# Performance work log

Measured on AMD Instinct MI355X. Metric: run time of the kernel, lower is better.

## Reference

```python
import jax, jax.numpy as jnp
import numpy as np

NODE, HIDDEN, BATCH, OUT, BUF = 200, 10, 50, 64, 500
DT = 0.0001
# ParamsJR('JR') defaults (all variances 0 -> constants, not Parameters)
A_, a_, B_, b_ = 3.25, 100.0, 22.0, 50.0
g_, c1_, c2_, c3_, c4_ = 1000.0, 135.0, 135.0 * 0.8, 135.0 * 0.25, 135.0 * 0.25
std_in_, vmax, v0, r_, y0, cy0 = 100.0, 5.0, 6.0, 0.56, 2.0, 5.0
LB, U_UB, NOISE_LB, SAT = 0.01, 500.0, 150.0, 1000.0


def setup_inputs() -> dict:
    key = jax.random.key(0)
    ks = jax.random.split(key, 8)
    inp = jax.random.normal(ks[0], (NODE, HIDDEN, BATCH), dtype=jnp.float32)
    noise_in = jax.random.normal(ks[1], (NODE, HIDDEN, BATCH), dtype=jnp.float32)
    hx = jax.random.uniform(ks[2], (NODE, 6), dtype=jnp.float32)
    hE = jax.random.uniform(ks[3], (NODE, BUF), dtype=jnp.float32)
    sc = jax.random.uniform(ks[4], (NODE, NODE), dtype=jnp.float32)
    w_bb = jax.random.uniform(ks[5], (NODE, NODE), dtype=jnp.float32)  # fitted gains (init 0.05 in torch)
    lm = jax.random.normal(ks[6], (OUT, NODE), dtype=jnp.float32)  # lead-field
    delays = jax.random.randint(ks[7], (NODE, NODE), 0, BUF)  # (dist/(1.5+relu(mu))).int64
    return {"inp": inp, "noise_in": noise_in, "hx": hx, "hE": hE,
            "sc": sc, "w_bb": w_bb, "lm": lm, "delays": delays}


def _sigmoid(x):
    return vmax / (1.0 + jnp.exp(r_ * (v0 - x)))


def _sys2nd(A, a, u, x, v):
    return A * a * u - 2.0 * a * v - a * a * x


def _forward(inp, noise_in, hx, hE, sc, w_bb, lm, delays):
    relu = jax.nn.relu
    A_e, a_e = relu(A_), 1.0 + relu(a_)          # 0*con+relu(A), 1*con+relu(a)
    B_e, b_e = relu(B_), 1.0 + relu(b_)
    g_e, c1e, c2e, c3e, c4e = (LB + relu(g_), LB + relu(c1_), LB + relu(c2_),
                               LB + relu(c3_), LB + relu(c4_))
    std_e = NOISE_LB + relu(std_in_)

    # normalized laplacian-style connectivity
    w = jnp.exp(w_bb) * sc
    wl = jnp.log1p(0.5 * (w + w.T))
    w_n = wl / jnp.linalg.norm(wl)
    dg = -jnp.diag(jnp.sum(w_n, axis=1))          # (node, node)
    rows = jnp.arange(NODE)[:, None]

    def step(carry, xs):
        M, E, I, Mv, Ev, Iv, hEb = carry
        u, noise = xs                              # (node,1) each
        Ed = hEb[rows, delays]                     # Ed[i,j] = hE[i, delays[i,j]]
        LEd = jnp.sum(w_n * Ed.T, axis=1, keepdims=True)  # (node,1)
        rM = _sigmoid(E - I)
        rE = (std_e * noise + g_e * (LEd + dg @ E)
              + c2e * _sigmoid(c1e * M))
        rI = c4e * _sigmoid(c3e * M)
        ddM = M + DT * Mv
        ddE = E + DT * Ev
        ddI = I + DT * Iv
        ddMv = Mv + DT * _sys2nd(A_e, a_e, u + U_UB * jnp.tanh(rM / U_UB), M, Mv)
        ddEv = Ev + DT * _sys2nd(A_e, a_e, U_UB * jnp.tanh(rE / U_UB), E, Ev)
        ddIv = Iv + DT * _sys2nd(B_e, b_e, U_UB * jnp.tanh(rI / U_UB), I, Iv)
        sat = lambda x: SAT * jnp.tanh(x / SAT)
        M, E, I, Mv, Ev, Iv = (sat(ddM), sat(ddE), sat(ddI),
                               sat(ddMv), sat(ddEv), sat(ddIv))
        hEb = jnp.concatenate([M, hEb[:, :-1]], axis=1)  # push pyramidal state into delay buffer
        return (M, E, I, Mv, Ev, Iv, hEb), None

    def tr_step(carry, xs):
        u_tr, n_tr = xs                            # (hidden, node, 1)
        carry, _ = jax.lax.scan(step, carry, (u_tr, n_tr))
        M, E, I, Mv, Ev, Iv, _ = carry
        return carry, (M[:, 0], E[:, 0], I[:, 0], Mv[:, 0], Ev[:, 0], Iv[:, 0])

    M, E, I = hx[:, 0:1], hx[:, 1:2], hx[:, 2:3]
    Mv, Ev, Iv = hx[:, 3:4], hx[:, 4:5], hx[:, 5:6]
    u_all = jnp.transpose(inp, (2, 1, 0))[..., None]       # (batch, hidden, node, 1)
    n_all = jnp.transpose(noise_in, (2, 1, 0))[..., None]
    carry, recs = jax.lax.scan(tr_step, (M, E, I, Mv, Ev, Iv, hE), (u_all, n_all))
    Mb, Eb, Ib, Mvb, Evb, Ivb = recs                       # (batch, node) each

    # lead-field: row-normalize then remove channel mean
    lm_n = lm / jnp.sqrt(jnp.sum(lm ** 2, axis=1, keepdims=True))
    lm_t = lm_n - jnp.mean(lm_n, axis=0, keepdims=True)
    eeg = cy0 * jnp.einsum('on,bn->ob', lm_t, Eb - Ib) - y0  # (output, batch)

    M, E, I, Mv, Ev, Iv, hEb = carry
    current_state = jnp.concatenate([M, E, I, Mv, Ev, Iv], axis=1)
    return eeg, current_state, Eb.T, Ib.T, Mb.T, Evb.T, Ivb.T, Mvb.T, hEb


def reference(inp, noise_in, hx, hE, sc, w_bb, lm, delays):
    return _forward(inp, noise_in, hx, hE, sc, w_bb, lm, delays)
```

## Files before the change

### kernel.cpp

```cpp
#include <hip/hip_runtime.h>
#include <math.h>

#define N_NODE 200
#define RING   512
#define ROWF   545
#define NSTEP  500
#define TB     32
#define NB     16
#define NWG    8
#define NTHR   256
#define JSL    25
#define NEARCAP 32
#define MDEP   36
#define MSZ    (MDEP * N_NODE)

#define FPBUF   (NWG * N_NODE * TB)
#define OFF_FP  0
#define OFF_BAR (2 * FPBUF)
#define WS_NEED ((size_t)(2 * FPBUF + 64) * 4)

#define SM_RED   0
#define SM_MREC  64
#define SM_US    28864
#define SM_NS    54464
#define SM_LED   80864
#define SM_RING  106464
#define SM_TOTAL 160964
#define SM_LMT   64
#define SM_DIFF  51264

__device__ __forceinline__ float ftanh(float x) {
    float ax = fabsf(x);
    float t  = __expf(-2.0f * ax);
    float r  = __fdividef(1.0f - t, 1.0f + t);
    return copysignf(r, x);
}
__device__ __forceinline__ float sigm(float x) {
    return __fdividef(5.0f, 1.0f + __expf(0.56f * (6.0f - x)));
}
__device__ __forceinline__ float satf(float x) {
    return 1000.0f * ftanh(x * 0.001f);
}

__device__ __forceinline__ void grid_barrier(int* slot, int nwg) {
    __syncthreads();
    if (threadIdx.x == 0) {
        __threadfence();
        __hip_atomic_fetch_add(slot, 1, __ATOMIC_ACQ_REL, __HIP_MEMORY_SCOPE_AGENT);
        while (__hip_atomic_load(slot, __ATOMIC_ACQUIRE, __HIP_MEMORY_SCOPE_AGENT) < nwg) {
            __builtin_amdgcn_s_sleep(2);
        }
        __threadfence();
    }
    __syncthreads();
}

__global__ void zero_bar(int* bar) {
    if (threadIdx.x < 64) bar[threadIdx.x] = 0;
}

__global__ __launch_bounds__(NTHR, 1)
void jansen_pg(const float* __restrict__ inp, const float* __restrict__ noise_in,
               const float* __restrict__ hx,  const float* __restrict__ hE,
               const float* __restrict__ sc,  const float* __restrict__ wbb,
               const float* __restrict__ lm,  const int*   __restrict__ delays,
               float* __restrict__ out, float* __restrict__ ws)
{
    __shared__ char smem[SM_TOTAL];
    double*   red  = (double*)(smem + SM_RED);
    float*    Mrec = (float*)(smem + SM_MREC);
    unsigned* n1OFF = (unsigned*)(smem + SM_US);
    float*    n1W   = (float*)(smem + SM_NS);
    unsigned* n0J   = (unsigned*)(smem + SM_LED);
    float*    n0W   = (float*)(smem + SM_LED + 8 * N_NODE * 4);
    float*    uS   = (float*)(smem + SM_US);
    float*    nS   = (float*)(smem + SM_NS);
    float*    LEdS = (float*)(smem + SM_LED);
    float*    ringS= (float*)(smem + SM_RING);

    const int tid = threadIdx.x;
    const int wg  = blockIdx.x;
    const int i   = tid;
    const int jlo = wg * JSL;

    float* fp  = ws + OFF_FP;
    int*   bar = (int*)(ws + OFF_BAR);

    double ssq = 0.0;
    for (int q = tid; q < N_NODE * N_NODE; q += NTHR) {
        int j = q / N_NODE, ii = q - j * N_NODE;
        float w1 = expf(wbb[ii * N_NODE + j]) * sc[ii * N_NODE + j];
        float w2 = expf(wbb[j * N_NODE + ii]) * sc[j * N_NODE + ii];
        float wl = log1pf(0.5f * (w1 + w2));
        ssq += (double)wl * (double)wl;
    }
    #pragma unroll
    for (int off = 32; off > 0; off >>= 1) ssq += __shfl_down(ssq, off, 64);
    if ((tid & 63) == 0) red[tid >> 6] = ssq;

    for (int p = tid; p < JSL * ROWF; p += NTHR) {
        int jl = p / ROWF, x = p - jl * ROWF;
        float v = 0.0f;
        if (x < 544) {
            int dd = (x < RING) ? (511 - x) : (1023 - x);
            if (dd < 500) v = hE[(jlo + jl) * 500 + dd];
        }
        ringS[p] = v;
    }
    for (int p = tid; p < MDEP * N_NODE; p += NTHR) {
        int s = p / N_NODE, j = p - s * N_NODE;
        Mrec[p] = (s >= 4) ? hE[j * 500 + (35 - s)] : 0.0f;
    }
    for (int p = tid; p < 32 * N_NODE; p += NTHR) {
        n1OFF[p] = 0u;
        n1W[p]   = 0.0f;
    }
    for (int p = tid; p < 8 * N_NODE; p += NTHR) {
        n0J[p] = 0u;
        n0W[p] = 0.0f;
    }
    __syncthreads();
    if (tid == 0) {
        double s = 0.0;
        #pragma unroll
        for (int r = 0; r < 8; ++r) s += red[r];
        red[0] = 1.0 / sqrt(s);
    }
    __syncthreads();
    const float inv = (float)red[0];

    float rowsum = 0.0f;
    float M = 0, E = 0, I = 0, Mvv = 0, Evv = 0, Ivv = 0;
    float wreg[JSL];
    int   ereg[JSL];
    #pragma unroll
    for (int jl = 0; jl < JSL; ++jl) { wreg[jl] = 0.0f; ereg[jl] = 0; }
    int cnt0 = 0, cnt1 = 0;
    if (i < N_NODE) {
        for (int j = 0; j < N_NODE; ++j) {
            float w1 = expf(wbb[i * N_NODE + j]) * sc[i * N_NODE + j];
            float w2 = expf(wbb[j * N_NODE + i]) * sc[j * N_NODE + i];
            float w  = log1pf(0.5f * (w1 + w2)) * inv;
            int d = delays[j * N_NODE + i];
            rowsum += w;
            if (d == 0) {
                if (cnt0 < 8) {
                    n0J[cnt0 * N_NODE + i] = (unsigned)j;
                    n0W[cnt0 * N_NODE + i] = w;
                    ++cnt0;
                }
            } else if (d < NEARCAP) {
                if (cnt1 < 32) {
                    n1OFF[cnt1 * N_NODE + i] = (unsigned)((35 - d) * N_NODE + j);
                    n1W  [cnt1 * N_NODE + i] = w;
                    ++cnt1;
                }
            }
        }
        #pragma unroll
        for (int jl = 0; jl < JSL; ++jl) {
            int j = jlo + jl;
            float w1 = expf(wbb[i * N_NODE + j]) * sc[i * N_NODE + j];
            float w2 = expf(wbb[j * N_NODE + i]) * sc[j * N_NODE + i];
            float w  = log1pf(0.5f * (w1 + w2)) * inv;
            int d = delays[j * N_NODE + i];
            wreg[jl] = (d < NEARCAP) ? 0.0f : w;
            ereg[jl] = 511 - d;
        }
        M   = hx[i * 6 + 0]; E   = hx[i * 6 + 1]; I   = hx[i * 6 + 2];
        Mvv = hx[i * 6 + 3]; Evv = hx[i * 6 + 4]; Ivv = hx[i * 6 + 5];
    }

    int   n1off[32]; float n1w[32];
    int   n0j[8];    float n0w[8];
    {
        const int ii = (i < N_NODE) ? i : 0;
        #pragma unroll
        for (int n = 0; n < 32; ++n) {
            n1off[n] = (int)n1OFF[n * N_NODE + ii];
            n1w[n]   = n1W[n * N_NODE + ii];
        }
        #pragma unroll
        for (int z = 0; z < 8; ++z) {
            n0j[z] = (int)n0J[z * N_NODE + ii];
            n0w[z] = n0W[z * N_NODE + ii];
        }
    }

    float LEdN = 0.0f;
    if (i < N_NODE) {
        float gA = 0.0f, gB = 0.0f, gC = 0.0f, gD = 0.0f;
        #pragma unroll
        for (int n = 0; n < 8; ++n) gA = fmaf(n1w[n], Mrec[n1off[n]], gA);
        if (cnt1 > 8) {
            #pragma unroll
            for (int n = 8; n < 16; ++n) gB = fmaf(n1w[n], Mrec[n1off[n]], gB);
        }
        if (cnt1 > 16) {
            #pragma unroll
            for (int n = 16; n < 24; ++n) gC = fmaf(n1w[n], Mrec[n1off[n]], gC);
        }
        if (cnt1 > 24) {
            #pragma unroll
            for (int n = 24; n < 32; ++n) gD = fmaf(n1w[n], Mrec[n1off[n]], gD);
        }
        LEdN = (gA + gB) + (gC + gD);
    }
    __syncthreads();

    int base36 = 0;
    for (int b = 0; b < NB; ++b) {
        const int t0 = b * TB;
        float* fpb = fp + (b & 1) * FPBUF;

        if (i < N_NODE) {
            float ac[TB];
            #pragma unroll
            for (int k = 0; k < TB; ++k) ac[k] = 0.0f;
            #pragma unroll
            for (int jl = 0; jl < JSL; ++jl) {
                float w  = wreg[jl];
                int   p0 = (t0 + ereg[jl]) & 511;
                const float* rb = ringS + jl * ROWF + p0;
                #pragma unroll
                for (int k = 0; k < TB; ++k)
                    ac[k] = fmaf(w, rb[k], ac[k]);
            }
            float4* fpw = (float4*)(fpb + wg * (N_NODE * TB) + i * TB);
            #pragma unroll
            for (int q = 0; q < 8; ++q)
                fpw[q] = make_float4(ac[4*q+0], ac[4*q+1], ac[4*q+2], ac[4*q+3]);

            #pragma unroll
            for (int k = 0; k < TB; ++k) {
                int t = t0 + k;
                float uv = 0.0f, nv = 0.0f;
                if (t < NSTEP) {
                    int bb = t / 10, h = t - 10 * bb;
                    uv = inp     [i * 500 + h * 50 + bb];
                    nv = noise_in[i * 500 + h * 50 + bb];
                }
                uS[k * N_NODE + i] = uv;
                nS[k * N_NODE + i] = nv;
            }
        }

        grid_barrier(bar + b, NWG);

        if (i < N_NODE) {
            const float* basep = fpb + i * TB;
            #pragma unroll
            for (int c = 0; c < 8; ++c) {
                float sx = 0, sy = 0, sz = 0, sw = 0;
                #pragma unroll
                for (int g = 0; g < NWG; ++g) {
                    float4 q = *(const float4*)(basep + g * (N_NODE * TB) + c * 4);
                    sx += q.x; sy += q.y; sz += q.z; sw += q.w;
                }
                LEdS[(c * 4 + 0) * N_NODE + i] = sx;
                LEdS[(c * 4 + 1) * N_NODE + i] = sy;
                LEdS[(c * 4 + 2) * N_NODE + i] = sz;
                LEdS[(c * 4 + 3) * N_NODE + i] = sw;
            }
        }
        __syncthreads();

        const int kmax = (NSTEP - t0 < TB) ? (NSTEP - t0) : TB;
        int bcur = t0 / 10, hcur = t0 - 10 * bcur;
        const bool ringw = (i >= jlo) && (i < jlo + JSL);
        const int  rbase = (i - jlo) * ROWF;
        for (int k = 0; k < kmax; ++k) {
            const int t = t0 + k;
            if (i < N_NODE) {
                const int base_prev = (base36 == 0) ? (MSZ - N_NODE) : (base36 - N_NODE);
                float LEd = LEdN + LEdS[k * N_NODE + i];
                float u  = uS[k * N_NODE + i];
                float nz = nS[k * N_NODE + i];
                #pragma unroll
                for (int z = 0; z < 4; ++z)
                    LEd = fmaf(n0w[z], Mrec[base_prev + n0j[z]], LEd);
                if (cnt0 > 4) {
                    #pragma unroll
                    for (int z = 4; z < 8; ++z)
                        LEd = fmaf(n0w[z], Mrec[base_prev + n0j[z]], LEd);
                }
                int base36n = base36 + N_NODE; if (base36n == MSZ) base36n = 0;
                float gA = 0.0f, gB = 0.0f, gC = 0.0f, gD = 0.0f;
                #pragma unroll
                for (int n = 0; n < 8; ++n) {
                    int a = base36n + n1off[n]; if (a >= MSZ) a -= MSZ;
                    gA = fmaf(n1w[n], Mrec[a], gA);
                }
                if (cnt1 > 8) {
                    #pragma unroll
                    for (int n = 8; n < 16; ++n) {
                        int a = base36n + n1off[n]; if (a >= MSZ) a -= MSZ;
                        gB = fmaf(n1w[n], Mrec[a], gB);
                    }
                }
                if (cnt1 > 16) {
                    #pragma unroll
                    for (int n = 16; n < 24; ++n) {
                        int a = base36n + n1off[n]; if (a >= MSZ) a -= MSZ;
                        gC = fmaf(n1w[n], Mrec[a], gC);
                    }
                }
                if (cnt1 > 24) {
                    #pragma unroll
                    for (int n = 24; n < 32; ++n) {
                        int a = base36n + n1off[n]; if (a >= MSZ) a -= MSZ;
                        gD = fmaf(n1w[n], Mrec[a], gD);
                    }
                }
                float rM = sigm(E - I);
                float rE = 250.0f * nz + 1000.01f * (LEd - rowsum * E) + 108.01f * sigm(135.01f * M);
                float rI = 33.76f * sigm(33.76f * M);
                float ddM = M + 1e-4f * Mvv;
                float ddE = E + 1e-4f * Evv;
                float ddI = I + 1e-4f * Ivv;
                float uu  = u + 500.0f * ftanh(rM * 0.002f);
                float ddMv = Mvv + 1e-4f * (328.25f * uu - 202.0f * Mvv - 10201.0f * M);
                float uE  = 500.0f * ftanh(rE * 0.002f);
                float ddEv = Evv + 1e-4f * (328.25f * uE - 202.0f * Evv - 10201.0f * E);
                float uI  = 500.0f * ftanh(rI * 0.002f);
                float ddIv = Ivv + 1e-4f * (1122.0f * uI - 102.0f * Ivv - 2601.0f * I);
                M   = satf(ddM);  E   = satf(ddE);  I   = satf(ddI);
                Mvv = satf(ddMv); Evv = satf(ddEv); Ivv = satf(ddIv);
                LEdN = (gA + gB) + (gC + gD);
                Mrec[base36 + i] = M;
                if (ringw) {
                    int pt = t & 511;
                    ringS[rbase + pt] = M;
                    if (pt < 32) ringS[rbase + pt + 512] = M;
                }
                if (wg == 0 && hcur == 9) {
                    out[ 4400 + i * 50 + bcur] = E;
                    out[14400 + i * 50 + bcur] = I;
                    out[24400 + i * 50 + bcur] = M;
                    out[34400 + i * 50 + bcur] = Evv;
                    out[44400 + i * 50 + bcur] = Ivv;
                    out[54400 + i * 50 + bcur] = Mvv;
                }
                ++hcur; if (hcur == 10) { hcur = 0; ++bcur; }
                base36 = base36n;
            }
            __syncthreads();
        }
    }

    for (int p = tid; p < JSL * 500; p += NTHR) {
        int jl = p / 500, dd = p - jl * 500;
        out[64400 + (jlo + jl) * 500 + dd] = ringS[jl * ROWF + ((499 - dd) & 511)];
    }
    if (wg != 0) return;

    if (i < N_NODE) {
        out[3200 + i * 6 + 0] = M;
        out[3200 + i * 6 + 1] = E;
        out[3200 + i * 6 + 2] = I;
        out[3200 + i * 6 + 3] = Mvv;
        out[3200 + i * 6 + 4] = Evv;
        out[3200 + i * 6 + 5] = Ivv;
    }

    float* lmt  = (float*)(smem + SM_LMT);
    float* diff = (float*)(smem + SM_DIFF);
    __syncthreads();
    if (tid < 64) {
        float s = 0.0f;
        for (int n = 0; n < N_NODE; ++n) { float v = lm[tid * N_NODE + n]; s += v * v; }
        float ivn = 1.0f / sqrtf(s);
        for (int n = 0; n < N_NODE; ++n) lmt[tid * N_NODE + n] = lm[tid * N_NODE + n] * ivn;
    }
    __syncthreads();
    if (tid < N_NODE) {
        float s = 0.0f;
        for (int o = 0; o < 64; ++o) s += lmt[o * N_NODE + tid];
        s *= (1.0f / 64.0f);
        for (int o = 0; o < 64; ++o) lmt[o * N_NODE + tid] -= s;
    }
    __syncthreads();
    for (int p = tid; p < 10000; p += NTHR) diff[p] = out[4400 + p] - out[14400 + p];
    __syncthreads();
    for (int p = tid; p < 3200; p += NTHR) {
        int o = p / 50, bb = p - o * 50;
        float s = 0.0f;
        for (int n = 0; n < N_NODE; ++n)
            s = fmaf(lmt[o * N_NODE + n], diff[n * 50 + bb], s);
        out[p] = 5.0f * s - 2.0f;
    }
}

__global__ __launch_bounds__(1024, 1)
void jansen_main(const float* __restrict__ inp, const float* __restrict__ noise_in,
                 const float* __restrict__ hx,  const float* __restrict__ hE,
                 const float* __restrict__ sc,  const float* __restrict__ wbb,
                 const float* __restrict__ lm,  const int*   __restrict__ delays,
                 float* __restrict__ out, float* __restrict__ ws)
{
    const int tid = threadIdx.x;
    const int i   = tid & 255;
    const int c   = tid >> 8;

    float* ring = ws;
    float* lmt  = ws + N_NODE * RING;

    __shared__ double red[18];
    __shared__ float  part[4][N_NODE];
    __shared__ float  wn[N_NODE * N_NODE];

    double ssq = 0.0;
    for (int p = tid; p < N_NODE * N_NODE; p += 1024) {
        int r0 = p / N_NODE;
        int cc = p - r0 * N_NODE;
        float w1 = expf(wbb[p]) * sc[p];
        float w2 = expf(wbb[cc * N_NODE + r0]) * sc[cc * N_NODE + r0];
        float v  = log1pf(0.5f * (w1 + w2));
        wn[p] = v;
        ssq += (double)v * (double)v;
    }
    #pragma unroll
    for (int off = 32; off > 0; off >>= 1) ssq += __shfl_down(ssq, off, 64);
    if ((tid & 63) == 0) red[tid >> 6] = ssq;
    __syncthreads();
    if (tid == 0) {
        double s = 0.0;
        for (int k = 0; k < 16; ++k) s += red[k];
        red[16] = 1.0 / sqrt(s);
    }
    __syncthreads();
    const float inv_norm = (float)red[16];
    for (int p = tid; p < N_NODE * N_NODE; p += 1024) wn[p] *= inv_norm;

    for (int p = tid; p < N_NODE * 500; p += 1024) {
        int j = p / 500, dd = p - j * 500;
        ring[j * RING + (511 - dd)] = hE[p];
    }
    if (tid < 64) {
        float s = 0.0f;
        for (int n = 0; n < N_NODE; ++n) { float v = lm[tid * N_NODE + n]; s += v * v; }
        float inv = 1.0f / sqrtf(s);
        for (int n = 0; n < N_NODE; ++n) lmt[tid * N_NODE + n] = lm[tid * N_NODE + n] * inv;
    }
    __syncthreads();
    if (tid < N_NODE) {
        float s = 0.0f;
        for (int o = 0; o < 64; ++o) s += lmt[o * N_NODE + tid];
        s *= (1.0f / 64.0f);
        for (int o = 0; o < 64; ++o) lmt[o * N_NODE + tid] -= s;
    }

    unsigned int dpk[25];
    if (i < N_NODE) {
        #pragma unroll
        for (int r0 = 0; r0 < 25; ++r0) {
            int d0 = delays[(c * 50 + 2 * r0    ) * N_NODE + i];
            int d1 = delays[(c * 50 + 2 * r0 + 1) * N_NODE + i];
            unsigned e0 = (unsigned)((-1 - d0) & 511);
            unsigned e1 = (unsigned)((-1 - d1) & 511);
            dpk[r0] = e0 | (e1 << 16);
        }
    }

    float M = 0, E = 0, I = 0, Mvv = 0, Evv = 0, Ivv = 0, rowsum = 0;
    if (c == 0 && i < N_NODE) {
        M   = hx[i * 6 + 0]; E   = hx[i * 6 + 1]; I   = hx[i * 6 + 2];
        Mvv = hx[i * 6 + 3]; Evv = hx[i * 6 + 4]; Ivv = hx[i * 6 + 5];
    }
    __syncthreads();
    if (c == 0 && i < N_NODE) {
        float s = 0.0f;
        for (int j = 0; j < N_NODE; ++j) s += wn[j * N_NODE + i];
        rowsum = s;
    }

    for (int t = 0; t < NSTEP; ++t) {
        if (i < N_NODE) {
            float acc = 0.0f;
            const float* ringc = ring + c * 50 * RING;
            const float* wnc   = wn + c * 50 * N_NODE + i;
            #pragma unroll
            for (int r0 = 0; r0 < 50; ++r0) {
                unsigned e = (dpk[r0 >> 1] >> ((r0 & 1) << 4)) & 0xffffu;
                int pos = (int)(((unsigned)t + e) & 511u);
                acc = fmaf(wnc[r0 * N_NODE], ringc[r0 * RING + pos], acc);
            }
            part[c][i] = acc;
        }
        __syncthreads();
        if (c == 0 && i < N_NODE) {
            float LEd = part[0][i] + part[1][i] + part[2][i] + part[3][i];
            int b = t / 10, h = t - b * 10;
            float u  = inp     [i * 500 + h * 50 + b];
            float nz = noise_in[i * 500 + h * 50 + b];
            float rM = 5.0f / (1.0f + expf(0.56f * (6.0f - (E - I))));
            float rE = 250.0f * nz + 1000.01f * (LEd - rowsum * E) + 108.01f * (5.0f / (1.0f + expf(0.56f * (6.0f - 135.01f * M))));
            float rI = 33.76f * (5.0f / (1.0f + expf(0.56f * (6.0f - 33.76f * M))));
            float ddM = M + 1e-4f * Mvv;
            float ddE = E + 1e-4f * Evv;
            float ddI = I + 1e-4f * Ivv;
            float uu  = u + 500.0f * tanhf(rM / 500.0f);
            float ddMv = Mvv + 1e-4f * (328.25f * uu - 202.0f * Mvv - 10201.0f * M);
            float uE  = 500.0f * tanhf(rE / 500.0f);
            float ddEv = Evv + 1e-4f * (328.25f * uE - 202.0f * Evv - 10201.0f * E);
            float uI  = 500.0f * tanhf(rI / 500.0f);
            float ddIv = Ivv + 1e-4f * (1122.0f * uI - 102.0f * Ivv - 2601.0f * I);
            M   = 1000.0f * tanhf(ddM / 1000.0f);
            E   = 1000.0f * tanhf(ddE / 1000.0f);
            I   = 1000.0f * tanhf(ddI / 1000.0f);
            Mvv = 1000.0f * tanhf(ddMv / 1000.0f);
            Evv = 1000.0f * tanhf(ddEv / 1000.0f);
            Ivv = 1000.0f * tanhf(ddIv / 1000.0f);
            ring[i * RING + (t & 511)] = M;
            if (h == 9) {
                out[ 4400 + i * 50 + b] = E;
                out[14400 + i * 50 + b] = I;
                out[24400 + i * 50 + b] = M;
                out[34400 + i * 50 + b] = Evv;
                out[44400 + i * 50 + b] = Ivv;
                out[54400 + i * 50 + b] = Mvv;
            }
        }
        __syncthreads();
    }

    if (c == 0 && i < N_NODE) {
        out[3200 + i * 6 + 0] = M;
        out[3200 + i * 6 + 1] = E;
        out[3200 + i * 6 + 2] = I;
        out[3200 + i * 6 + 3] = Mvv;
        out[3200 + i * 6 + 4] = Evv;
        out[3200 + i * 6 + 5] = Ivv;
    }
    for (int p = tid; p < N_NODE * 500; p += 1024) {
        int ii = p / 500, dd = p - ii * 500;
        out[64400 + p] = ring[ii * RING + (499 - dd)];
    }
    __syncthreads();
    for (int p = tid; p < 64 * 50; p += 1024) {
        int o = p / 50, b = p - o * 50;
        float s = 0.0f;
        for (int n = 0; n < N_NODE; ++n)
            s += lmt[o * N_NODE + n] * (out[4400 + n * 50 + b] - out[14400 + n * 50 + b]);
        out[p] = 5.0f * s - 2.0f;
    }
}

extern "C" void kernel_launch(void* const* d_in, const int* in_sizes, int n_in,
                              void* d_out, int out_size, void* d_ws, size_t ws_size,
                              hipStream_t stream) {
    if (ws_size >= WS_NEED) {
        zero_bar<<<1, 64, 0, stream>>>((int*)((float*)d_ws + OFF_BAR));
        jansen_pg<<<NWG, NTHR, 0, stream>>>(
            (const float*)d_in[0], (const float*)d_in[1], (const float*)d_in[2],
            (const float*)d_in[3], (const float*)d_in[4], (const float*)d_in[5],
            (const float*)d_in[6], (const int*)d_in[7],
            (float*)d_out, (float*)d_ws);
    } else {
        jansen_main<<<1, 1024, 0, stream>>>(
            (const float*)d_in[0], (const float*)d_in[1], (const float*)d_in[2],
            (const float*)d_in[3], (const float*)d_in[4], (const float*)d_in[5],
            (const float*)d_in[6], (const int*)d_in[7],
            (float*)d_out, (float*)d_ws);
    }
}
```

Before: 1.253 ms.

## Advance two timesteps per block barrier by recomputing zero-delay neighbor states locally

The inner time loop now runs two ODE steps between consecutive __syncthreads instead of one. For step t+1, the zero-delay neighbor term needs neighbor M at step t. That value is rebuilt locally as satf(M + 1e-4*Mv) from last-step M and Mv values kept in small shared double buffers, and the near-delay gathers for both steps are interleaved. The input and noise staging arrays are packed into float2, and the norm reduction now sums only the 4 wavefront partials that exist. This halves block synchronisations per step, at the cost of redundant neighbor recomputation and higher register pressure.

```diff
diff --git a/kernel.cpp b/kernel.cpp
--- a/kernel.cpp
+++ b/kernel.cpp
@@ -10,24 +10,30 @@
 #define NWG    8
 #define NTHR   256
 #define JSL    25
-#define NEARCAP 32
 #define MDEP   36
 #define MSZ    (MDEP * N_NODE)
+#define L1CAP  32
+#define L0CAP  8
 
 #define FPBUF   (NWG * N_NODE * TB)
 #define OFF_FP  0
 #define OFF_BAR (2 * FPBUF)
 #define WS_NEED ((size_t)(2 * FPBUF + 64) * 4)
 
-#define SM_RED   0
-#define SM_MREC  64
-#define SM_US    28864
-#define SM_NS    54464
-#define SM_LED   80864
-#define SM_RING  106464
-#define SM_TOTAL 160964
-#define SM_LMT   64
-#define SM_DIFF  51264
+#define SM_RED    0
+#define SM_MREC   64
+#define SM_MLAST  28864
+#define SM_MVLAST 30464
+#define SM_US     32064
+#define SM_LEDS   83264
+#define SM_RING   108864
+#define SM_TOTAL  163364
+#define SM_N1X    SM_US
+#define SM_N1W    (SM_US + 25600)
+#define SM_N0J    SM_LEDS
+#define SM_N0W    (SM_LEDS + 6400)
+#define SM_LMT    64
+#define SM_DIFF   51264
 
 __device__ __forceinline__ float ftanh(float x) {
     float ax = fabsf(x);
@@ -59,23 +65,41 @@
     if (threadIdx.x < 64) bar[threadIdx.x] = 0;
 }
 
+#define ODE_STEP(LEDV, UV, NZV) do { \
+    float rM = sigm(E - I); \
+    float rE = 250.0f * (NZV) + 1000.01f * ((LEDV) - rowsum * E) + 108.01f * sigm(135.01f * M); \
+    float rI = 33.76f * sigm(33.76f * M); \
+    float ddM = fmaf(1e-4f, Mvv, M); \
+    float ddE = fmaf(1e-4f, Evv, E); \
+    float ddI = fmaf(1e-4f, Ivv, I); \
+    float uu  = (UV) + 500.0f * ftanh(rM * 0.002f); \
+    float ddMv = Mvv + 1e-4f * (328.25f * uu - 202.0f * Mvv - 10201.0f * M); \
+    float uE  = 500.0f * ftanh(rE * 0.002f); \
+    float ddEv = Evv + 1e-4f * (328.25f * uE - 202.0f * Evv - 10201.0f * E); \
+    float uI  = 500.0f * ftanh(rI * 0.002f); \
+    float ddIv = Ivv + 1e-4f * (1122.0f * uI - 102.0f * Ivv - 2601.0f * I); \
+    M   = satf(ddM);  E   = satf(ddE);  I   = satf(ddI); \
+    Mvv = satf(ddMv); Evv = satf(ddEv); Ivv = satf(ddIv); \
+} while (0)
+
 __global__ __launch_bounds__(NTHR, 1)
-void jansen_pg(const float* __restrict__ inp, const float* __restrict__ noise_in,
+void jansen_2s(const float* __restrict__ inp, const float* __restrict__ noise_in,
                const float* __restrict__ hx,  const float* __restrict__ hE,
                const float* __restrict__ sc,  const float* __restrict__ wbb,
                const float* __restrict__ lm,  const int*   __restrict__ delays,
                float* __restrict__ out, float* __restrict__ ws)
 {
     __shared__ char smem[SM_TOTAL];
-    double*   red  = (double*)(smem + SM_RED);
-    float*    Mrec = (float*)(smem + SM_MREC);
-    unsigned* n1OFF = (unsigned*)(smem + SM_US);
-    float*    n1W   = (float*)(smem + SM_NS);
-    unsigned* n0J   = (unsigned*)(smem + SM_LED);
-    float*    n0W   = (float*)(smem + SM_LED + 8 * N_NODE * 4);
-    float*    uS   = (float*)(smem + SM_US);
-    float*    nS   = (float*)(smem + SM_NS);
-    float*    LEdS = (float*)(smem + SM_LED);
+    double*   red   = (double*)(smem + SM_RED);
+    float*    Mrec  = (float*)(smem + SM_MREC);
+    float*    Mlast = (float*)(smem + SM_MLAST);
+    float*    Mvlast= (float*)(smem + SM_MVLAST);
+    unsigned* n1X = (unsigned*)(smem + SM_N1X);
+    float*    n1W = (float*)(smem + SM_N1W);
+    unsigned* n0J = (unsigned*)(smem + SM_N0J);
+    float*    n0W = (float*)(smem + SM_N0W);
+    float2*   unS  = (float2*)(smem + SM_US);
+    float*    LEdS = (float*)(smem + SM_LEDS);
     float*    ringS= (float*)(smem + SM_RING);
 
     const int tid = threadIdx.x;
@@ -107,23 +131,17 @@
         }
         ringS[p] = v;
     }
-    for (int p = tid; p < MDEP * N_NODE; p += NTHR) {
+    for (int p = tid; p < MSZ; p += NTHR) {
         int s = p / N_NODE, j = p - s * N_NODE;
         Mrec[p] = (s >= 4) ? hE[j * 500 + (35 - s)] : 0.0f;
     }
-    for (int p = tid; p < 32 * N_NODE; p += NTHR) {
-        n1OFF[p] = 0u;
-        n1W[p]   = 0.0f;
-    }
-    for (int p = tid; p < 8 * N_NODE; p += NTHR) {
-        n0J[p] = 0u;
-        n0W[p] = 0.0f;
-    }
+    for (int p = tid; p < L1CAP * N_NODE; p += NTHR) { n1X[p] = 0u; n1W[p] = 0.0f; }
+    for (int p = tid; p < L0CAP * N_NODE; p += NTHR) { n0J[p] = 0u; n0W[p] = 0.0f; }
     __syncthreads();
     if (tid == 0) {
         double s = 0.0;
         #pragma unroll
-        for (int r = 0; r < 8; ++r) s += red[r];
+        for (int r = 0; r < 4; ++r) s += red[r];
         red[0] = 1.0 / sqrt(s);
     }
     __syncthreads();
@@ -144,15 +162,15 @@
             int d = delays[j * N_NODE + i];
             rowsum += w;
             if (d == 0) {
-                if (cnt0 < 8) {
+                if (cnt0 < L0CAP) {
                     n0J[cnt0 * N_NODE + i] = (unsigned)j;
                     n0W[cnt0 * N_NODE + i] = w;
                     ++cnt0;
                 }
-            } else if (d < NEARCAP) {
-                if (cnt1 < 32) {
-                    n1OFF[cnt1 * N_NODE + i] = (unsigned)((35 - d) * N_NODE + j);
-                    n1W  [cnt1 * N_NODE + i] = w;
+            } else if (d < 32) {
+                if (cnt1 < L1CAP) {
+                    n1X[cnt1 * N_NODE + i] = (unsigned)((35 - d) * N_NODE + j);
+                    n1W[cnt1 * N_NODE + i] = w;
                     ++cnt1;
                 }
             }
@@ -164,51 +182,32 @@
             float w2 = expf(wbb[j * N_NODE + i]) * sc[j * N_NODE + i];
             float w  = log1pf(0.5f * (w1 + w2)) * inv;
             int d = delays[j * N_NODE + i];
-            wreg[jl] = (d < NEARCAP) ? 0.0f : w;
+            wreg[jl] = (d < 32) ? 0.0f : w;
             ereg[jl] = 511 - d;
         }
         M   = hx[i * 6 + 0]; E   = hx[i * 6 + 1]; I   = hx[i * 6 + 2];
         Mvv = hx[i * 6 + 3]; Evv = hx[i * 6 + 4]; Ivv = hx[i * 6 + 5];
-    }
-
-    int   n1off[32]; float n1w[32];
-    int   n0j[8];    float n0w[8];
+        Mlast [N_NODE + i] = M;
+        Mvlast[N_NODE + i] = Mvv;
+    }
+
+    int   n1off[L1CAP]; float n1w[L1CAP];
+    int   l0j[L0CAP];   float l0w[L0CAP];
     {
         const int ii = (i < N_NODE) ? i : 0;
         #pragma unroll
-        for (int n = 0; n < 32; ++n) {
-            n1off[n] = (int)n1OFF[n * N_NODE + ii];
+        for (int n = 0; n < L1CAP; ++n) {
+            n1off[n] = (int)n1X[n * N_NODE + ii];
             n1w[n]   = n1W[n * N_NODE + ii];
         }
         #pragma unroll
-        for (int z = 0; z < 8; ++z) {
-            n0j[z] = (int)n0J[z * N_NODE + ii];
-            n0w[z] = n0W[z * N_NODE + ii];
-        }
-    }
-
-    float LEdN = 0.0f;
-    if (i < N_NODE) {
-        float gA = 0.0f, gB = 0.0f, gC = 0.0f, gD = 0.0f;
-        #pragma unroll
-        for (int n = 0; n < 8; ++n) gA = fmaf(n1w[n], Mrec[n1off[n]], gA);
-        if (cnt1 > 8) {
-            #pragma unroll
-            for (int n = 8; n < 16; ++n) gB = fmaf(n1w[n], Mrec[n1off[n]], gB);
-        }
-        if (cnt1 > 16) {
-            #pragma unroll
-            for (int n = 16; n < 24; ++n) gC = fmaf(n1w[n], Mrec[n1off[n]], gC);
-        }
-        if (cnt1 > 24) {
-            #pragma unroll
-            for (int n = 24; n < 32; ++n) gD = fmaf(n1w[n], Mrec[n1off[n]], gD);
-        }
-        LEdN = (gA + gB) + (gC + gD);
-    }
-    __syncthreads();
-
-    int base36 = 0;
+        for (int z = 0; z < L0CAP; ++z) {
+            l0j[z] = (int)n0J[z * N_NODE + ii];
+            l0w[z] = n0W[z * N_NODE + ii];
+        }
+    }
+    __syncthreads();
+
     for (int b = 0; b < NB; ++b) {
         const int t0 = b * TB;
         float* fpb = fp + (b & 1) * FPBUF;
@@ -240,8 +239,7 @@
                     uv = inp     [i * 500 + h * 50 + bb];
                     nv = noise_in[i * 500 + h * 50 + bb];
                 }
-                uS[k * N_NODE + i] = uv;
-                nS[k * N_NODE + i] = nv;
+                unS[k * N_NODE + i] = make_float2(uv, nv);
             }
         }
 
@@ -266,72 +264,75 @@
         __syncthreads();
 
         const int kmax = (NSTEP - t0 < TB) ? (NSTEP - t0) : TB;
+        int s36 = t0 % MDEP;
         int bcur = t0 / 10, hcur = t0 - 10 * bcur;
         const bool ringw = (i >= jlo) && (i < jlo + JSL);
         const int  rbase = (i - jlo) * ROWF;
-        for (int k = 0; k < kmax; ++k) {
-            const int t = t0 + k;
+        for (int k2 = 0; k2 < kmax; k2 += 2) {
+            const int t = t0 + k2;
             if (i < N_NODE) {
-                const int base_prev = (base36 == 0) ? (MSZ - N_NODE) : (base36 - N_NODE);
-                float LEd = LEdN + LEdS[k * N_NODE + i];
-                float u  = uS[k * N_NODE + i];
-                float nz = nS[k * N_NODE + i];
-                #pragma unroll
-                for (int z = 0; z < 4; ++z)
-                    LEd = fmaf(n0w[z], Mrec[base_prev + n0j[z]], LEd);
-                if (cnt0 > 4) {
-                    #pragma unroll
-                    for (int z = 4; z < 8; ++z)
-                        LEd = fmaf(n0w[z], Mrec[base_prev + n0j[z]], LEd);
-                }
-                int base36n = base36 + N_NODE; if (base36n == MSZ) base36n = 0;
-                float gA = 0.0f, gB = 0.0f, gC = 0.0f, gD = 0.0f;
+                const int base  = s36 * N_NODE;
+                int basen = base + N_NODE; if (basen >= MSZ) basen -= MSZ;
+                const int pp = (((t >> 1) + 1) & 1) * N_NODE;
+                const int cp = ((t >> 1) & 1) * N_NODE;
+                float a0 = LEdS[k2 * N_NODE + i],       a1 = 0.f, a2 = 0.f, a3 = 0.f;
+                float b0 = LEdS[(k2 + 1) * N_NODE + i], b1 = 0.f, b2 = 0.f, b3 = 0.f;
                 #pragma unroll
                 for (int n = 0; n < 8; ++n) {
-                    int a = base36n + n1off[n]; if (a >= MSZ) a -= MSZ;
-                    gA = fmaf(n1w[n], Mrec[a], gA);
+                    int aa = base  + n1off[n]; if (aa >= MSZ) aa -= MSZ;
+                    int ab = basen + n1off[n]; if (ab >= MSZ) ab -= MSZ;
+                    a0 = fmaf(n1w[n], Mrec[aa], a0);
+                    b0 = fmaf(n1w[n], Mrec[ab], b0);
                 }
                 if (cnt1 > 8) {
                     #pragma unroll
                     for (int n = 8; n < 16; ++n) {
-                        int a = base36n + n1off[n]; if (a >= MSZ) a -= MSZ;
-                        gB = fmaf(n1w[n], Mrec[a], gB);
+                        int aa = base  + n1off[n]; if (aa >= MSZ) aa -= MSZ;
+                        int ab = basen + n1off[n]; if (ab >= MSZ) ab -= MSZ;
+                        a1 = fmaf(n1w[n], Mrec[aa], a1);
+                        b1 = fmaf(n1w[n], Mrec[ab], b1);
                     }
                 }
                 if (cnt1 > 16) {
                     #pragma unroll
                     for (int n = 16; n < 24; ++n) {
-                        int a = base36n + n1off[n]; if (a >= MSZ) a -= MSZ;
-                        gC = fmaf(n1w[n], Mrec[a], gC);
+                        int aa = base  + n1off[n]; if (aa >= MSZ) aa -= MSZ;
+                        int ab = basen + n1off[n]; if (ab >= MSZ) ab -= MSZ;
+                        a2 = fmaf(n1w[n], Mrec[aa], a2);
+                        b2 = fmaf(n1w[n], Mrec[ab], b2);
                     }
                 }
                 if (cnt1 > 24) {
                     #pragma unroll
                     for (int n = 24; n < 32; ++n) {
-                        int a = base36n + n1off[n]; if (a >= MSZ) a -= MSZ;
-                        gD = fmaf(n1w[n], Mrec[a], gD);
+                        int aa = base  + n1off[n]; if (aa >= MSZ) aa -= MSZ;
+                        int ab = basen + n1off[n]; if (ab >= MSZ) ab -= MSZ;
+                        a3 = fmaf(n1w[n], Mrec[aa], a3);
+                        b3 = fmaf(n1w[n], Mrec[ab], b3);
                     }
                 }
-                float rM = sigm(E - I);
-                float rE = 250.0f * nz + 1000.01f * (LEd - rowsum * E) + 108.01f * sigm(135.01f * M);
-                float rI = 33.76f * sigm(33.76f * M);
-                float ddM = M + 1e-4f * Mvv;
-                float ddE = E + 1e-4f * Evv;
-                float ddI = I + 1e-4f * Ivv;
-                float uu  = u + 500.0f * ftanh(rM * 0.002f);
-                float ddMv = Mvv + 1e-4f * (328.25f * uu - 202.0f * Mvv - 10201.0f * M);
-                float uE  = 500.0f * ftanh(rE * 0.002f);
-                float ddEv = Evv + 1e-4f * (328.25f * uE - 202.0f * Evv - 10201.0f * E);
-                float uI  = 500.0f * ftanh(rI * 0.002f);
-                float ddIv = Ivv + 1e-4f * (1122.0f * uI - 102.0f * Ivv - 2601.0f * I);
-                M   = satf(ddM);  E   = satf(ddE);  I   = satf(ddI);
-                Mvv = satf(ddMv); Evv = satf(ddEv); Ivv = satf(ddIv);
-                LEdN = (gA + gB) + (gC + gD);
-                Mrec[base36 + i] = M;
-                if (ringw) {
+                #pragma unroll
+                for (int z = 0; z < L0CAP; ++z) {
+                    if (cnt0 > z) {
+                        int aa = base + 35 * N_NODE + l0j[z]; if (aa >= MSZ) aa -= MSZ;
+                        a0 = fmaf(l0w[z], Mrec[aa], a0);
+                        float mj = satf(fmaf(1e-4f, Mvlast[pp + l0j[z]], Mlast[pp + l0j[z]]));
+                        b0 = fmaf(l0w[z], mj, b0);
+                    }
+                }
+                float LEdA = (a0 + a1) + (a2 + a3);
+                float LEdB = (b0 + b1) + (b2 + b3);
+                float2 unA = unS[k2 * N_NODE + i];
+                float2 unB = unS[(k2 + 1) * N_NODE + i];
+
+                ODE_STEP(LEdA, unA.x, unA.y);
+                Mrec[base + i] = M;
+                {
                     int pt = t & 511;
-                    ringS[rbase + pt] = M;
-                    if (pt < 32) ringS[rbase + pt + 512] = M;
+                    if (ringw) {
+                        ringS[rbase + pt] = M;
+                        if (pt < 32) ringS[rbase + pt + 512] = M;
+                    }
                 }
                 if (wg == 0 && hcur == 9) {
                     out[ 4400 + i * 50 + bcur] = E;
@@ -342,9 +343,31 @@
                     out[54400 + i * 50 + bcur] = Mvv;
                 }
                 ++hcur; if (hcur == 10) { hcur = 0; ++bcur; }
-                base36 = base36n;
+
+                ODE_STEP(LEdB, unB.x, unB.y);
+                Mrec[basen + i] = M;
+                {
+                    int pt = (t + 1) & 511;
+                    if (ringw) {
+                        ringS[rbase + pt] = M;
+                        if (pt < 32) ringS[rbase + pt + 512] = M;
+                    }
+                }
+                if (wg == 0 && hcur == 9) {
+                    out[ 4400 + i * 50 + bcur] = E;
+                    out[14400 + i * 50 + bcur] = I;
+                    out[24400 + i * 50 + bcur] = M;
+                    out[34400 + i * 50 + bcur] = Evv;
+                    out[44400 + i * 50 + bcur] = Ivv;
+                    out[54400 + i * 50 + bcur] = Mvv;
+                }
+                ++hcur; if (hcur == 10) { hcur = 0; ++bcur; }
+
+                Mlast [cp + i] = M;
+                Mvlast[cp + i] = Mvv;
             }
             __syncthreads();
+            s36 += 2; if (s36 >= MDEP) s36 -= MDEP;
         }
     }
 
@@ -551,7 +574,7 @@
                               hipStream_t stream) {
     if (ws_size >= WS_NEED) {
         zero_bar<<<1, 64, 0, stream>>>((int*)((float*)d_ws + OFF_BAR));
-        jansen_pg<<<NWG, NTHR, 0, stream>>>(
+        jansen_2s<<<NWG, NTHR, 0, stream>>>(
             (const float*)d_in[0], (const float*)d_in[1], (const float*)d_in[2],
             (const float*)d_in[3], (const float*)d_in[4], (const float*)d_in[5],
             (const float*)d_in[6], (const int*)d_in[7],
```

After: 1.284 ms. 1.02x slower.
